# Kernel tuning notes

Measured on AMD Instinct MI355X. Metric: run time of the kernel, lower is better.

The kernel has to match this reference:

```python
import jax, jax.numpy as jnp
import numpy as np

NEG_INF = -9e15


def setup_inputs() -> dict:
    key = jax.random.key(0)
    k1, k2, k3, k4 = jax.random.split(key, 4)
    N, F_in, H, F_out = 4096, 512, 8, 64
    node_features = jax.random.normal(k1, (N, F_in), dtype=jnp.float32)
    adj_matrix = jax.random.randint(k2, (N, N), 0, 2, dtype=jnp.int32)
    # ensure self-loops so every row has at least one unmasked entry
    adj_matrix = jnp.maximum(adj_matrix, jnp.eye(N, dtype=jnp.int32))
    W = jax.random.normal(k3, (H, F_in, F_out), dtype=jnp.float32) * 0.05
    a = jax.random.normal(k4, (H, 2 * F_out), dtype=jnp.float32) * 0.05
    return {"node_features": node_features, "adj_matrix": adj_matrix, "W": W, "a": a}


def reference(node_features, adj_matrix, W, a):
    alpha = 0.2
    H, F_in, F_out = W.shape
    # Per-head linear projection: [H, N, F_out]
    Wh = jnp.einsum("nf,hfo->hno", node_features, W)
    # Attention logits e_ij = LeakyReLU(a1 . Wh_i + a2 . Wh_j)
    f_src = jnp.einsum("hno,ho->hn", Wh, a[:, :F_out])   # [H, N]
    f_dst = jnp.einsum("hno,ho->hn", Wh, a[:, F_out:])   # [H, N]
    e = jax.nn.leaky_relu(f_src[:, :, None] + f_dst[:, None, :], negative_slope=alpha)  # [H, N, N]
    # Mask by adjacency, softmax over neighbors
    masked = jnp.where(adj_matrix[None, :, :] > 0, e, NEG_INF)
    attn = jax.nn.softmax(masked, axis=-1)               # [H, N, N]
    # Aggregate neighbor features per head
    h_prime = jnp.einsum("hnm,hmo->hno", attn, Wh)       # [H, N, F_out]
    # Concat heads along feature dim -> [N, H*F_out]
    return jnp.transpose(h_prime, (1, 0, 2)).reshape(h_prime.shape[1], H * F_out)
```

## Files before the change

kernel.cpp:

```cpp
#include <hip/hip_runtime.h>
#include <stdint.h>


#define NN 4096
#define FIN 512
#define NH 8
#define FO 64

typedef _Float16 f16x8 __attribute__((ext_vector_type(8)));
typedef _Float16 f16x2 __attribute__((ext_vector_type(2)));
typedef __attribute__((ext_vector_type(4))) float f32x4;

union H8 { f16x8 v; f16x2 p[4]; unsigned u[4]; };
union U2 { unsigned u; f16x2 v; };

__device__ __forceinline__ unsigned short f2h(float f) {
  _Float16 h = (_Float16)f;
  return __builtin_bit_cast(unsigned short, h);
}

__global__ __launch_bounds__(256) void prep_kernel(
    const float* __restrict__ X, const int* __restrict__ adj, const float* __restrict__ W,
    const float* __restrict__ a,
    unsigned short* __restrict__ Xh, unsigned short* __restrict__ WbT,
    unsigned* __restrict__ adjbitsT, unsigned short* __restrict__ WAh) {
  int bid = blockIdx.x, tid = threadIdx.x;
  if (bid < 2048) {
    int item = bid * 256 + tid;
    int jt = item >> 12, r = item & 4095;
    const int* p = adj + (size_t)r * NN + jt * 32;
    unsigned bits = 0;
#pragma unroll
    for (int b = 0; b < 32; b += 4) {
      int4 v = *(const int4*)(p + b);
      bits |= (unsigned)(v.x & 1) << b;
      bits |= (unsigned)(v.y & 1) << (b + 1);
      bits |= (unsigned)(v.z & 1) << (b + 2);
      bits |= (unsigned)(v.w & 1) << (b + 3);
    }
    adjbitsT[item] = bits;
  } else if (bid < 4096) {
    int item = (bid - 2048) * 256 + tid;
    float4 v = ((const float4*)X)[item];
    ushort4 o;
    o.x = f2h(v.x); o.y = f2h(v.y); o.z = f2h(v.z); o.w = f2h(v.w);
    ((ushort4*)Xh)[item] = o;
  } else if (bid < 5120) {
    int item = (bid - 4096) * 256 + tid;
    int o = item & 63, k = (item >> 6) & 511, h = item >> 15;
    WbT[h * 32768 + o * 512 + k] = f2h(W[h * 32768 + k * 64 + o]);
  } else {
    int item = (bid - 5120) * 256 + tid;
    int h = item >> 10, which = (item >> 9) & 1, k = item & 511;
    const float4* wp = (const float4*)(W + ((size_t)h * FIN + k) * FO);
    const float4* ap = (const float4*)(a + h * 128 + which * 64);
    float s = 0.f;
#pragma unroll
    for (int o4 = 0; o4 < 16; ++o4) {
      float4 w4 = wp[o4], a4 = ap[o4];
      s += w4.x * a4.x + w4.y * a4.y + w4.z * a4.z + w4.w * a4.w;
    }
    WAh[(h * 2 + which) * FIN + k] = f2h(s);
  }
}

__global__ __launch_bounds__(512, 4) void proj_sd_kernel(
    const unsigned short* __restrict__ Xh, const unsigned short* __restrict__ WbT,
    const unsigned short* __restrict__ WAh,
    unsigned short* __restrict__ Whfrag, float* __restrict__ Rf,
    unsigned short* __restrict__ E1h, unsigned short* __restrict__ E2h) {
  __shared__ float red[4 * 64 * 20];
  int lane = threadIdx.x & 63, wave = threadIdx.x >> 6;
  int row16 = lane & 15, grp = lane >> 4;
  int bx = blockIdx.x;
  if (bx >= 512) {
    int i0 = ((bx - 512) * 8 + wave) * 16;
    if (i0 >= NN) return;
    f32x4 acc = {0, 0, 0, 0};
    const unsigned short* xb = Xh + (size_t)(i0 + row16) * FIN + grp * 8;
    const unsigned short* wb = WAh + row16 * FIN + grp * 8;
#pragma unroll
    for (int k0 = 0; k0 < FIN; k0 += 32)
      acc = __builtin_amdgcn_mfma_f32_16x16x32_f16(*(const f16x8*)(xb + k0),
                                                   *(const f16x8*)(wb + k0), acc, 0, 0, 0);
    int hh = row16 >> 1;
#pragma unroll
    for (int reg = 0; reg < 4; ++reg) {
      int rr = i0 + grp * 4 + reg;
      float v = acc[reg];
      if (row16 & 1) {
        E1h[hh * NN + rr] = f2h(0.5f * __expf(v));
        E2h[hh * NN + rr] = f2h(0.5f * __expf(0.2f * v));
      } else {
        Rf[hh * NN + rr] = __expf(-0.8f * v);
      }
    }
    return;
  }
  int kh = wave >> 2, jb = wave & 3;
  int job = bx * 4 + jb;
  int h = job & 7, rt = job >> 3;
  int i0 = rt * 16;
  f32x4 acc[4] = {{0,0,0,0},{0,0,0,0},{0,0,0,0},{0,0,0,0}};
  const unsigned short* xb = Xh + (size_t)(i0 + row16) * FIN + kh * 256 + grp * 8;
  const unsigned short* wb = WbT + h * (FO * FIN) + row16 * FIN + kh * 256 + grp * 8;
#pragma unroll
  for (int k0 = 0; k0 < 256; k0 += 32) {
    f16x8 af = *(const f16x8*)(xb + k0);
#pragma unroll
    for (int cb = 0; cb < 4; ++cb)
      acc[cb] = __builtin_amdgcn_mfma_f32_16x16x32_f16(
          af, *(const f16x8*)(wb + cb * 16 * FIN + k0), acc[cb], 0, 0, 0);
  }
  if (kh == 1) {
    float* q = red + (jb * 64 + lane) * 20;
#pragma unroll
    for (int cb = 0; cb < 4; ++cb) *(f32x4*)(q + cb * 4) = acc[cb];
  }
  __syncthreads();
  if (kh == 0) {
    const float* q = red + (jb * 64 + lane) * 20;
#pragma unroll
    for (int cb = 0; cb < 4; ++cb) acc[cb] += *(const f32x4*)(q + cb * 4);
    int jt = i0 >> 5;
    int kk0 = (i0 & 31) + grp * 4;
    int tl = (kk0 >> 3) * 16 + row16;
    int e0 = kk0 & 7;
#pragma unroll
    for (int cb = 0; cb < 4; ++cb) {
      ushort4 pk;
      pk.x = f2h(acc[cb][0]); pk.y = f2h(acc[cb][1]);
      pk.z = f2h(acc[cb][2]); pk.w = f2h(acc[cb][3]);
      *(ushort4*)(Whfrag + (((size_t)h * 128 + jt) * 4 + cb) * 512 + tl * 8 + e0) = pk;
    }
  }
}

struct Tile {
  f16x8 b0, b1, b2, b3;
  f16x8 e1, e2;
  unsigned aw0, aw1, aw2, aw3;
};

__global__ __launch_bounds__(256, 2) void gat_kernel(
    const unsigned* __restrict__ adjbitsT, const unsigned short* __restrict__ Whfrag,
    const float* __restrict__ Rf, const unsigned short* __restrict__ E1h,
    const unsigned short* __restrict__ E2h, float* __restrict__ out) {
  __shared__ __align__(16) float red[3072];
  int h = blockIdx.y;
  int lane = threadIdx.x & 63, jseg = threadIdx.x >> 6;
  int row16 = lane & 15, grp = lane >> 4;
  int r0 = blockIdx.x * 64;
  int jt0 = jseg * 32;

  f16x2 Rh[4];
#pragma unroll
  for (int gi = 0; gi < 4; ++gi) {
    _Float16 rv = (_Float16)Rf[h * NN + r0 + gi * 16 + row16];
    Rh[gi][0] = rv; Rh[gi][1] = rv;
  }

  H8 ones;
#pragma unroll
  for (int k = 0; k < 4; ++k) ones.u[k] = 0x3C003C00u;

  const unsigned short* wsrc = Whfrag + (size_t)h * 262144 + (size_t)jt0 * 2048 + lane * 8;
  const unsigned short* e1p = E1h + h * NN + jt0 * 32 + grp * 8;
  const unsigned short* e2p = E2h + h * NN + jt0 * 32 + grp * 8;
  const unsigned* ap = adjbitsT + (size_t)jt0 * NN + r0 + row16;

  f32x4 acc[4][5];
#pragma unroll
  for (int gi = 0; gi < 4; ++gi)
#pragma unroll
    for (int cc = 0; cc < 5; ++cc) acc[gi][cc] = (f32x4){0, 0, 0, 0};

  auto ld = [&](int p, Tile& t) {
    const unsigned short* bs = wsrc + (size_t)p * 2048;
    t.b0 = *(const f16x8*)(bs);
    t.b1 = *(const f16x8*)(bs + 512);
    t.b2 = *(const f16x8*)(bs + 1024);
    t.b3 = *(const f16x8*)(bs + 1536);
    t.e1 = *(const f16x8*)(e1p + p * 32);
    t.e2 = *(const f16x8*)(e2p + p * 32);
    const unsigned* aq = ap + (size_t)p * NN;
    t.aw0 = aq[0]; t.aw1 = aq[16]; t.aw2 = aq[32]; t.aw3 = aq[48];
  };

  auto compute = [&](const Tile& t) {
    H8 e1, e2;
    e1.v = t.e1; e2.v = t.e2;
    unsigned aw[4] = {t.aw0, t.aw1, t.aw2, t.aw3};
#pragma unroll
    for (int gi = 0; gi < 4; ++gi) {
      unsigned bb = (aw[gi] >> (grp * 8)) & 0xffu;
      unsigned tt = bb | (bb << 15);
      H8 af;
#pragma unroll
      for (int k = 0; k < 4; ++k) {
        f16x2 mx = __builtin_elementwise_max(e1.p[k], Rh[gi] * e2.p[k]);
        U2 m;
        m.u = (tt << (14 - 2 * k)) & 0x40004000u;
        af.p[k] = mx * m.v;
      }
      acc[gi][0] = __builtin_amdgcn_mfma_f32_16x16x32_f16(af.v, t.b0, acc[gi][0], 0, 0, 0);
      acc[gi][1] = __builtin_amdgcn_mfma_f32_16x16x32_f16(af.v, t.b1, acc[gi][1], 0, 0, 0);
      acc[gi][2] = __builtin_amdgcn_mfma_f32_16x16x32_f16(af.v, t.b2, acc[gi][2], 0, 0, 0);
      acc[gi][3] = __builtin_amdgcn_mfma_f32_16x16x32_f16(af.v, t.b3, acc[gi][3], 0, 0, 0);
      acc[gi][4] = __builtin_amdgcn_mfma_f32_16x16x32_f16(af.v, ones.v, acc[gi][4], 0, 0, 0);
    }
  };

  Tile tA, tB;
  ld(0, tA);
#pragma unroll 1
  for (int p2 = 0; p2 < 15; ++p2) {
    ld(2 * p2 + 1, tB);
    asm volatile("" ::: "memory");
    compute(tA);
    ld(2 * p2 + 2, tA);
    asm volatile("" ::: "memory");
    compute(tB);
  }
  ld(31, tB);
  compute(tA);
  compute(tB);

  __syncthreads();
#pragma unroll
  for (int cc = 0; cc < 5; ++cc) {
    if (jseg != 0) {
#pragma unroll
      for (int gi = 0; gi < 4; ++gi)
        *(f32x4*)(red + (((jseg - 1) * 4 + gi) * 64 + lane) * 4) = acc[gi][cc];
    }
    __syncthreads();
    if (jseg == 0) {
#pragma unroll
      for (int s = 0; s < 3; ++s)
#pragma unroll
        for (int gi = 0; gi < 4; ++gi)
          acc[gi][cc] += *(const f32x4*)(red + ((s * 4 + gi) * 64 + lane) * 4);
    }
    __syncthreads();
  }

  if (jseg == 0) {
#pragma unroll
    for (int gi = 0; gi < 4; ++gi) {
#pragma unroll
      for (int reg = 0; reg < 4; ++reg) {
        float inv = 1.0f / acc[gi][4][reg];
        int row = r0 + gi * 16 + grp * 4 + reg;
        float* op = out + (size_t)row * (NH * FO) + h * FO + row16;
        op[0]  = acc[gi][0][reg] * inv;
        op[16] = acc[gi][1][reg] * inv;
        op[32] = acc[gi][2][reg] * inv;
        op[48] = acc[gi][3][reg] * inv;
      }
    }
  }
}

extern "C" void kernel_launch(void* const* d_in, const int* in_sizes, int n_in,
                              void* d_out, int out_size, void* d_ws, size_t ws_size,
                              hipStream_t stream) {
  const float* X  = (const float*)d_in[0];
  const int* adj  = (const int*)d_in[1];
  const float* W  = (const float*)d_in[2];
  const float* a  = (const float*)d_in[3];
  float* out = (float*)d_out;
  char* ws = (char*)d_ws;

  unsigned short* Xh     = (unsigned short*)(ws + 0);
  unsigned short* WbT    = (unsigned short*)(ws + 4194304);
  unsigned* adjbitsT     = (unsigned*)(ws + 4718592);
  unsigned short* Whfrag = (unsigned short*)(ws + 6815744);
  unsigned short* WAh    = (unsigned short*)(ws + 11010048);
  float* Rf              = (float*)(ws + 11026432);
  unsigned short* E1h    = (unsigned short*)(ws + 11288576);
  unsigned short* E2h    = (unsigned short*)(ws + 11354112);

  prep_kernel<<<5152, 256, 0, stream>>>(X, adj, W, a, Xh, WbT, adjbitsT, WAh);
  proj_sd_kernel<<<544, 512, 0, stream>>>(Xh, WbT, WAh, Whfrag, Rf, E1h, E2h);
  gat_kernel<<<dim3(64, 8), 256, 0, stream>>>(adjbitsT, Whfrag, Rf, E1h, E2h, out);
}
```

Measured before the change: 77.90 us.

## Fuse X fp16 conversion into projection and move adjacency packing alongside it

Drops the separate X-to-fp16 pass and converts fp32 X to fp16 on the fly inside the projection MFMA loads. The adjacency bit-packing moves from the prep kernel into the projection kernel as extra blocks, so the heavy adjacency read (64 MB of int32) can run concurrently with the projection work. The prep kernel now handles only the W transforms, which shortens the chain before the projection and removes the Xh buffer. In exchange, X is read as fp32 several times (once per head job) instead of as fp16, roughly doubling projection load traffic.

```diff
diff --git a/kernel.cpp b/kernel.cpp
--- a/kernel.cpp
+++ b/kernel.cpp
@@ -19,14 +19,49 @@
   return __builtin_bit_cast(unsigned short, h);
 }
 
-__global__ __launch_bounds__(256) void prep_kernel(
-    const float* __restrict__ X, const int* __restrict__ adj, const float* __restrict__ W,
-    const float* __restrict__ a,
-    unsigned short* __restrict__ Xh, unsigned short* __restrict__ WbT,
-    unsigned* __restrict__ adjbitsT, unsigned short* __restrict__ WAh) {
+__device__ __forceinline__ f16x8 ld_cvt8(const float* p) {
+  float4 a = *(const float4*)p, b = *(const float4*)(p + 4);
+  f16x8 r;
+  r[0] = (_Float16)a.x; r[1] = (_Float16)a.y; r[2] = (_Float16)a.z; r[3] = (_Float16)a.w;
+  r[4] = (_Float16)b.x; r[5] = (_Float16)b.y; r[6] = (_Float16)b.z; r[7] = (_Float16)b.w;
+  return r;
+}
+
+__global__ __launch_bounds__(256) void prep_w_kernel(
+    const float* __restrict__ W, const float* __restrict__ a,
+    unsigned short* __restrict__ WbT, unsigned short* __restrict__ WAh) {
   int bid = blockIdx.x, tid = threadIdx.x;
-  if (bid < 2048) {
+  if (bid < 1024) {
     int item = bid * 256 + tid;
+    int o = item & 63, k = (item >> 6) & 511, h = item >> 15;
+    WbT[h * 32768 + o * 512 + k] = f2h(W[h * 32768 + k * 64 + o]);
+  } else {
+    int item = (bid - 1024) * 256 + tid;
+    int h = item >> 10, which = (item >> 9) & 1, k = item & 511;
+    const float4* wp = (const float4*)(W + ((size_t)h * FIN + k) * FO);
+    const float4* ap = (const float4*)(a + h * 128 + which * 64);
+    float s = 0.f;
+#pragma unroll
+    for (int o4 = 0; o4 < 16; ++o4) {
+      float4 w4 = wp[o4], a4 = ap[o4];
+      s += w4.x * a4.x + w4.y * a4.y + w4.z * a4.z + w4.w * a4.w;
+    }
+    WAh[(h * 2 + which) * FIN + k] = f2h(s);
+  }
+}
+
+__global__ __launch_bounds__(512, 4) void proj_adj_kernel(
+    const float* __restrict__ X, const int* __restrict__ adj,
+    const unsigned short* __restrict__ WbT, const unsigned short* __restrict__ WAh,
+    unsigned short* __restrict__ Whfrag, float* __restrict__ Rf,
+    unsigned short* __restrict__ E1h, unsigned short* __restrict__ E2h,
+    unsigned* __restrict__ adjbitsT) {
+  __shared__ float red[4 * 64 * 20];
+  int lane = threadIdx.x & 63, wave = threadIdx.x >> 6;
+  int row16 = lane & 15, grp = lane >> 4;
+  int bx = blockIdx.x;
+  if (bx >= 544) {
+    int item = (bx - 544) * 512 + threadIdx.x;
     int jt = item >> 12, r = item & 4095;
     const int* p = adj + (size_t)r * NN + jt * 32;
     unsigned bits = 0;
@@ -39,49 +74,17 @@
       bits |= (unsigned)(v.w & 1) << (b + 3);
     }
     adjbitsT[item] = bits;
-  } else if (bid < 4096) {
-    int item = (bid - 2048) * 256 + tid;
-    float4 v = ((const float4*)X)[item];
-    ushort4 o;
-    o.x = f2h(v.x); o.y = f2h(v.y); o.z = f2h(v.z); o.w = f2h(v.w);
-    ((ushort4*)Xh)[item] = o;
-  } else if (bid < 5120) {
-    int item = (bid - 4096) * 256 + tid;
-    int o = item & 63, k = (item >> 6) & 511, h = item >> 15;
-    WbT[h * 32768 + o * 512 + k] = f2h(W[h * 32768 + k * 64 + o]);
-  } else {
-    int item = (bid - 5120) * 256 + tid;
-    int h = item >> 10, which = (item >> 9) & 1, k = item & 511;
-    const float4* wp = (const float4*)(W + ((size_t)h * FIN + k) * FO);
-    const float4* ap = (const float4*)(a + h * 128 + which * 64);
-    float s = 0.f;
-#pragma unroll
-    for (int o4 = 0; o4 < 16; ++o4) {
-      float4 w4 = wp[o4], a4 = ap[o4];
-      s += w4.x * a4.x + w4.y * a4.y + w4.z * a4.z + w4.w * a4.w;
-    }
-    WAh[(h * 2 + which) * FIN + k] = f2h(s);
-  }
-}
-
-__global__ __launch_bounds__(512, 4) void proj_sd_kernel(
-    const unsigned short* __restrict__ Xh, const unsigned short* __restrict__ WbT,
-    const unsigned short* __restrict__ WAh,
-    unsigned short* __restrict__ Whfrag, float* __restrict__ Rf,
-    unsigned short* __restrict__ E1h, unsigned short* __restrict__ E2h) {
-  __shared__ float red[4 * 64 * 20];
-  int lane = threadIdx.x & 63, wave = threadIdx.x >> 6;
-  int row16 = lane & 15, grp = lane >> 4;
-  int bx = blockIdx.x;
+    return;
+  }
   if (bx >= 512) {
     int i0 = ((bx - 512) * 8 + wave) * 16;
     if (i0 >= NN) return;
     f32x4 acc = {0, 0, 0, 0};
-    const unsigned short* xb = Xh + (size_t)(i0 + row16) * FIN + grp * 8;
+    const float* xb = X + (size_t)(i0 + row16) * FIN + grp * 8;
     const unsigned short* wb = WAh + row16 * FIN + grp * 8;
 #pragma unroll
     for (int k0 = 0; k0 < FIN; k0 += 32)
-      acc = __builtin_amdgcn_mfma_f32_16x16x32_f16(*(const f16x8*)(xb + k0),
+      acc = __builtin_amdgcn_mfma_f32_16x16x32_f16(ld_cvt8(xb + k0),
                                                    *(const f16x8*)(wb + k0), acc, 0, 0, 0);
     int hh = row16 >> 1;
 #pragma unroll
@@ -102,11 +105,11 @@
   int h = job & 7, rt = job >> 3;
   int i0 = rt * 16;
   f32x4 acc[4] = {{0,0,0,0},{0,0,0,0},{0,0,0,0},{0,0,0,0}};
-  const unsigned short* xb = Xh + (size_t)(i0 + row16) * FIN + kh * 256 + grp * 8;
+  const float* xb = X + (size_t)(i0 + row16) * FIN + kh * 256 + grp * 8;
   const unsigned short* wb = WbT + h * (FO * FIN) + row16 * FIN + kh * 256 + grp * 8;
 #pragma unroll
   for (int k0 = 0; k0 < 256; k0 += 32) {
-    f16x8 af = *(const f16x8*)(xb + k0);
+    f16x8 af = ld_cvt8(xb + k0);
 #pragma unroll
     for (int cb = 0; cb < 4; ++cb)
       acc[cb] = __builtin_amdgcn_mfma_f32_16x16x32_f16(
@@ -272,16 +275,16 @@
   float* out = (float*)d_out;
   char* ws = (char*)d_ws;
 
-  unsigned short* Xh     = (unsigned short*)(ws + 0);
-  unsigned short* WbT    = (unsigned short*)(ws + 4194304);
-  unsigned* adjbitsT     = (unsigned*)(ws + 4718592);
-  unsigned short* Whfrag = (unsigned short*)(ws + 6815744);
-  unsigned short* WAh    = (unsigned short*)(ws + 11010048);
-  float* Rf              = (float*)(ws + 11026432);
-  unsigned short* E1h    = (unsigned short*)(ws + 11288576);
-  unsigned short* E2h    = (unsigned short*)(ws + 11354112);
-
-  prep_kernel<<<5152, 256, 0, stream>>>(X, adj, W, a, Xh, WbT, adjbitsT, WAh);
-  proj_sd_kernel<<<544, 512, 0, stream>>>(Xh, WbT, WAh, Whfrag, Rf, E1h, E2h);
+  unsigned short* WbT    = (unsigned short*)(ws + 0);
+  unsigned* adjbitsT     = (unsigned*)(ws + 524288);
+  unsigned short* Whfrag = (unsigned short*)(ws + 2621440);
+  unsigned short* WAh    = (unsigned short*)(ws + 6815744);
+  float* Rf              = (float*)(ws + 6832128);
+  unsigned short* E1h    = (unsigned short*)(ws + 6963200);
+  unsigned short* E2h    = (unsigned short*)(ws + 7028736);
+
+  prep_w_kernel<<<1056, 256, 0, stream>>>(W, a, WbT, WAh);
+  proj_adj_kernel<<<1568, 512, 0, stream>>>(X, adj, WbT, WAh, Whfrag, Rf, E1h, E2h,
+                                            adjbitsT);
   gat_kernel<<<dim3(64, 8), 256, 0, stream>>>(adjbitsT, Whfrag, Rf, E1h, E2h, out);
 }
```

Measured after the change: 77.20 us. About the same (-0.9%).
